# Performance work log

Measured on AMD Instinct MI355X. Metric: run time of the kernel, lower is better.

The kernel has to match this reference:

```python
import jax, jax.numpy as jnp
import numpy as np

DIM = 1024
HEADS = 16


def setup_inputs() -> dict:
    key = jax.random.key(0)
    ks = jax.random.split(key, 9)
    B, N, C = 2, 2048, DIM
    hd = C // HEADS
    s = 1.0 / np.sqrt(C)
    x = jax.random.normal(ks[0], (B, N, C), dtype=jnp.float32)
    wq = jax.random.normal(ks[1], (C, C), dtype=jnp.float32) * s
    wk = jax.random.normal(ks[2], (C, C), dtype=jnp.float32) * s
    wv = jax.random.normal(ks[3], (C, C), dtype=jnp.float32) * s
    wp = jax.random.normal(ks[4], (C, C), dtype=jnp.float32) * s
    bp = jnp.zeros((C,), dtype=jnp.float32)
    # rotary table: angles theta_j = 10000^{-2j/hd}, positions 0..N-1
    inv_freq = 1.0 / (10000.0 ** (jnp.arange(0, hd, 2, dtype=jnp.float32) / hd))
    ang = jnp.arange(N, dtype=jnp.float32)[:, None] * inv_freq[None, :]  # (N, hd//2)
    cos = jnp.cos(ang)
    sin = jnp.sin(ang)
    return {"x": x, "wq": wq, "wk": wk, "wv": wv, "wp": wp, "bp": bp,
            "cos": cos, "sin": sin, "num_heads": HEADS}


def _apply_rotary(t, cos, sin):
    # t: (B, N, H, D); cos/sin: (N, D//2) -> broadcast (1, N, 1, D//2)
    B, N, H, D = t.shape
    tr = t.reshape(B, N, H, D // 2, 2)
    t1, t2 = tr[..., 0], tr[..., 1]
    c = cos[None, :, None, :]
    s = sin[None, :, None, :]
    o1 = t1 * c - t2 * s
    o2 = t1 * s + t2 * c
    return jnp.stack([o1, o2], axis=-1).reshape(B, N, H, D)


def reference(x, wq, wk, wv, wp, bp, cos, sin, num_heads):
    B, N, C = x.shape
    H = num_heads
    D = C // H
    q = (x @ wq.T).reshape(B, N, H, D)
    k = (x @ wk.T).reshape(B, N, H, D)
    v = (x @ wv.T).reshape(B, N, H, D)
    q = _apply_rotary(q, cos, sin)
    k = _apply_rotary(k, cos, sin)
    scale = 1.0 / jnp.sqrt(jnp.asarray(D, dtype=x.dtype))
    # scores: (B, H, N, N)
    scores = jnp.einsum('bnhd,bmhd->bhnm', q, k) * scale
    attn = jax.nn.softmax(scores, axis=-1)
    out = jnp.einsum('bhnm,bmhd->bnhd', attn, v).reshape(B, N, C)
    return out @ wp.T + bp
```

## Files before the change

kernel.cpp:

```cpp
#include <hip/hip_runtime.h>
#include <hip/hip_bf16.h>
#include <stdint.h>

#define DEVI __device__ __forceinline__

using bf16 = __hip_bfloat16;
typedef __bf16 bf16x8 __attribute__((ext_vector_type(8)));
typedef __bf16 bf16x4 __attribute__((ext_vector_type(4)));
typedef float f32x4 __attribute__((ext_vector_type(4)));
typedef float f32x16 __attribute__((ext_vector_type(16)));
typedef int i32x2 __attribute__((ext_vector_type(2)));

static constexpr int Bb = 2, Nn = 2048, Cc = 1024, Hh = 16, Dd = 64;
static constexpr float CSC = 0.125f * 1.44269504088896340736f;

DEVI bf16 f2bf(float x) {
  __bf16 h = (__bf16)x;
  return *(bf16*)&h;
}
DEVI float fexp2(float x) { return __builtin_amdgcn_exp2f(x); }

DEVI bf16x8 cvt8(f32x4 a, f32x4 b) {
  bf16x8 r;
  r[0] = (__bf16)a[0]; r[1] = (__bf16)a[1]; r[2] = (__bf16)a[2]; r[3] = (__bf16)a[3];
  r[4] = (__bf16)b[0]; r[5] = (__bf16)b[1]; r[6] = (__bf16)b[2]; r[7] = (__bf16)b[3];
  return r;
}

DEVI uint32_t pk2(float a, float b) {
  __bf16 x = (__bf16)a, y = (__bf16)b;
  uint16_t ux = *(uint16_t*)&x, uy = *(uint16_t*)&y;
  return (uint32_t)ux | ((uint32_t)uy << 16);
}

DEVI bf16x8 mk8(uint32_t a, uint32_t b, uint32_t c, uint32_t d) {
  union { uint32_t u[4]; bf16x8 v; } x;
  x.u[0] = a; x.u[1] = b; x.u[2] = c; x.u[3] = d;
  return x.v;
}

DEVI void gld_lds16(const bf16* g, bf16* l) {
  __builtin_amdgcn_global_load_lds(
      (__attribute__((address_space(1))) void*)(g),
      (__attribute__((address_space(3))) void*)(l),
      16, 0, 0);
}

__global__ __launch_bounds__(256) void k_cvt(const float* __restrict__ x,
                                             const float* __restrict__ wq,
                                             const float* __restrict__ wk,
                                             const float* __restrict__ wv,
                                             const float* __restrict__ wp,
                                             bf16* xb, bf16* wqb, bf16* wkb,
                                             bf16* wvb, bf16* wpb) {
  int bid = blockIdx.x;
  const float* src; bf16* dst; size_t off;
  if (bid < 2048) {
    src = x; dst = xb; off = (size_t)bid * 2048;
  } else {
    int s = (bid - 2048) >> 9, r = (bid - 2048) & 511;
    off = (size_t)r * 2048;
    src = s == 0 ? wq : s == 1 ? wk : s == 2 ? wv : wp;
    dst = s == 0 ? wqb : s == 1 ? wkb : s == 2 ? wvb : wpb;
  }
  size_t i = off + (size_t)threadIdx.x * 8;
  f32x4 a = *(const f32x4*)(src + i);
  f32x4 b = *(const f32x4*)(src + i + 4);
  *(bf16x8*)(dst + i) = cvt8(a, b);
}

template <int MFC, class Epi>
DEVI void gemm_dbuf(const bf16* __restrict__ A, const bf16* __restrict__ Bw,
                    int K, int m0, int n0, bf16* lA, bf16* lB, Epi epi) {
  constexpr int BM = MFC * 32;
  constexpr int PA = BM / 64;
  constexpr int ASZ = BM * 32, BSZ = 128 * 32;
  const int t = threadIdx.x;
  const int lane = t & 63, wave = t >> 6, g = lane >> 4;
  const int wr = wave >> 1, wc = wave & 1;

  auto stage = [&](int k0, int buf) {
#pragma unroll
    for (int p = 0; p < PA; ++p) {
      int c = p * 256 + t;
      gld_lds16(A + (size_t)(m0 + (c >> 2)) * K + k0 + (c & 3) * 8,
                lA + buf * ASZ + (size_t)(p * 256 + wave * 64) * 8);
    }
#pragma unroll
    for (int p = 0; p < 2; ++p) {
      int c = p * 256 + t;
      gld_lds16(Bw + (size_t)(n0 + (c >> 2)) * K + k0 + (c & 3) * 8,
                lB + buf * BSZ + (size_t)(p * 256 + wave * 64) * 8);
    }
  };

  f32x4 acc[MFC][4] = {};
  stage(0, 0);
  __syncthreads();

  const int NS = K / 32;
  for (int s = 0; s < NS; ++s) {
    const int cur = s & 1;
    if (s + 1 < NS) stage((s + 1) * 32, cur ^ 1);

    bf16x8 aF[MFC];
#pragma unroll
    for (int mf = 0; mf < MFC; ++mf)
      aF[mf] = *(const bf16x8*)(lA + cur * ASZ +
                                (wr * (BM / 2) + mf * 16 + (lane & 15)) * 32 + g * 8);
#pragma unroll
    for (int nf = 0; nf < 4; ++nf) {
      bf16x8 bF = *(const bf16x8*)(lB + cur * BSZ +
                                   (wc * 64 + nf * 16 + (lane & 15)) * 32 + g * 8);
#pragma unroll
      for (int mf = 0; mf < MFC; ++mf)
        acc[mf][nf] = __builtin_amdgcn_mfma_f32_16x16x32_bf16(aF[mf], bF, acc[mf][nf], 0, 0, 0);
    }
    __syncthreads();
  }

#pragma unroll
  for (int mf = 0; mf < MFC; ++mf)
#pragma unroll
    for (int nf = 0; nf < 4; ++nf)
#pragma unroll
      for (int r = 0; r < 4; ++r) {
        int gm = m0 + wr * (BM / 2) + mf * 16 + g * 4 + r;
        int gn = n0 + wc * 64 + nf * 16 + (lane & 15);
        epi(gm, gn, acc[mf][nf][r]);
      }
}

struct EpiRope {
  bf16* dst; const float* cosw; const float* sinw; float scale;
  DEVI void operator()(int gm, int gn, float v) const {
    int b = gm >> 11, n = gm & 2047;
    int h = gn >> 6, d = gn & 63;
    int i = d >> 1;
    float c = cosw[n * 32 + i], s = sinw[n * 32 + i];
    float p = __shfl_xor(v, 1);
    float o = (d & 1) ? (p * s + v * c) : (v * c - p * s);
    dst[((size_t)(b * Hh + h) * Nn + n) * 64 + d] = f2bf(o * scale);
  }
};

struct EpiVt {
  bf16* dst;
  DEVI void operator()(int gm, int gn, float v) const {
    int h = gm >> 6, d = gm & 63;
    int b = gn >> 11, n = gn & 2047;
    dst[((size_t)(b * Hh + h) * 64 + d) * Nn + n] = f2bf(v);
  }
};

struct EpiProj {
  float* dst; const float* bias;
  DEVI void operator()(int gm, int gn, float v) const {
    dst[(size_t)gm * Cc + gn] = v + bias[gn];
  }
};

__global__ __launch_bounds__(256) void k_qkv(const bf16* __restrict__ xb,
                                             const bf16* __restrict__ wqb,
                                             const bf16* __restrict__ wkb,
                                             const bf16* __restrict__ wvb,
                                             bf16* q_ws, bf16* k_ws, bf16* vt_ws,
                                             const float* __restrict__ cw,
                                             const float* __restrict__ sw) {
  __shared__ __align__(16) bf16 lA[2 * 128 * 32];
  __shared__ __align__(16) bf16 lB[2 * 128 * 32];
  int bid = blockIdx.x;
  if (bid < 512) {
    int sub = bid & 255;
    int m0 = (sub >> 3) * 128, n0 = (sub & 7) * 128;
    bool isq = bid < 256;
    gemm_dbuf<4>(xb, isq ? wqb : wkb, Cc, m0, n0, lA, lB,
                 EpiRope{isq ? q_ws : k_ws, cw, sw, isq ? CSC : 1.0f});
  } else {
    int sub = bid - 512;
    int m0 = (sub & 7) * 128, n0 = (sub >> 3) * 128;
    gemm_dbuf<4>(wvb, xb, Cc, m0, n0, lA, lB, EpiVt{vt_ws});
  }
}

__global__ __launch_bounds__(256) void k_proj(const bf16* __restrict__ A,
                                              const bf16* __restrict__ W,
                                              float* dst, const float* __restrict__ bias) {
  __shared__ __align__(16) bf16 lA[2 * 64 * 32];
  __shared__ __align__(16) bf16 lB[2 * 128 * 32];
  gemm_dbuf<2>(A, W, Cc, blockIdx.x * 64, blockIdx.y * 128, lA, lB,
               EpiProj{dst, bias});
}

__global__ __launch_bounds__(256) void k_flash(const bf16* __restrict__ q_ws,
                                               const bf16* __restrict__ k_ws,
                                               const bf16* __restrict__ vt_ws,
                                               bf16* __restrict__ attn_o) {
  __shared__ __align__(16) bf16 lK[2][64 * 64];
  __shared__ __align__(16) bf16 lV[2][64 * 64];

  const int t = threadIdx.x, lane = t & 63, wave = t >> 6;
  const int l31 = lane & 31, hi = lane >> 5;
  const int bh = blockIdx.y;
  const int q0w = blockIdx.x * 128 + wave * 32;
  const bf16* qg = q_ws + (size_t)bh * Nn * 64;
  const bf16* kg = k_ws + (size_t)bh * Nn * 64;
  const bf16* vg = vt_ws + (size_t)bh * 64 * Nn;

  bf16x8 qF[4];
#pragma unroll
  for (int kd = 0; kd < 4; ++kd)
    qF[kd] = *(const bf16x8*)(qg + (size_t)(q0w + l31) * 64 + kd * 16 + hi * 8);

  f32x16 accO[2] = {};
  float LsL = 0.f;

  auto stage_tile = [&](int kt, int buf) {
#pragma unroll
    for (int p = 0; p < 2; ++p) {
      int c = p * 256 + t;
      int row = c >> 3, cis = (c & 7) ^ (row & 7);
      gld_lds16(kg + (size_t)(kt * 64 + row) * 64 + cis * 8,
                lK[buf] + (size_t)(p * 256 + wave * 64) * 8);
      gld_lds16(vg + (size_t)row * Nn + kt * 64 + cis * 8,
                lV[buf] + (size_t)(p * 256 + wave * 64) * 8);
    }
  };

  stage_tile(0, 0);
  __syncthreads();

  constexpr int NT = Nn / 64;
  for (int kt = 0; kt < NT; ++kt) {
    const int cur = kt & 1;
    if (kt + 1 < NT) stage_tile(kt + 1, cur ^ 1);

#pragma unroll
    for (int kb = 0; kb < 2; ++kb) {
      f32x16 accT = {};
      __builtin_amdgcn_s_setprio(1);
#pragma unroll
      for (int kd = 0; kd < 4; ++kd) {
        int row = kb * 32 + l31;
        bf16x8 kF = *(const bf16x8*)(lK[cur] +
            ((row * 64 + kd * 16 + hi * 8) ^ ((row & 7) << 3)));
        accT = __builtin_amdgcn_mfma_f32_32x32x16_bf16(kF, qF[kd], accT, 0, 0, 0);
      }
      __builtin_amdgcn_s_setprio(0);

      float p[16];
#pragma unroll
      for (int r = 0; r < 16; ++r) { p[r] = fexp2(accT[r]); LsL += p[r]; }

      uint32_t c01 = pk2(p[0], p[1]),  c23 = pk2(p[2], p[3]);
      uint32_t c89 = pk2(p[4], p[5]),  cab = pk2(p[6], p[7]);
      uint32_t d01 = pk2(p[8], p[9]),  d23 = pk2(p[10], p[11]);
      uint32_t d89 = pk2(p[12], p[13]), dab = pk2(p[14], p[15]);
      i32x2 s0a = __builtin_amdgcn_permlane32_swap((int)c01, (int)c89, false, false);
      i32x2 s0b = __builtin_amdgcn_permlane32_swap((int)c23, (int)cab, false, false);
      i32x2 s1a = __builtin_amdgcn_permlane32_swap((int)d01, (int)d89, false, false);
      i32x2 s1b = __builtin_amdgcn_permlane32_swap((int)d23, (int)dab, false, false);
      bf16x8 paF[2] = { mk8(s0a[0], s0b[0], s0a[1], s0b[1]),
                        mk8(s1a[0], s1b[0], s1a[1], s1b[1]) };

      __builtin_amdgcn_s_setprio(1);
#pragma unroll
      for (int d0 = 0; d0 < 2; ++d0) {
#pragma unroll
        for (int s = 0; s < 2; ++s) {
          int vrow = d0 * 32 + l31;
          bf16x8 vF = *(const bf16x8*)(lV[cur] +
              ((vrow * 64 + kb * 32 + s * 16 + hi * 8) ^ ((vrow & 7) << 3)));
          accO[d0] = __builtin_amdgcn_mfma_f32_32x32x16_bf16(paF[s], vF, accO[d0], 0, 0, 0);
        }
      }
      __builtin_amdgcn_s_setprio(0);
    }

    __syncthreads();
  }

  float L = LsL + __shfl_xor(LsL, 32);

  const int b = bh >> 4, h = bh & 15;
#pragma unroll
  for (int r = 0; r < 16; ++r) {
    int ql = (r & 3) + 8 * (r >> 2) + 4 * hi;
    float inv = 1.0f / __shfl(L, ql);
    int qrow = q0w + ql;
#pragma unroll
    for (int d0 = 0; d0 < 2; ++d0) {
      int d = d0 * 32 + l31;
      attn_o[((size_t)(b * Nn + qrow)) * Cc + h * 64 + d] = f2bf(accO[d0][r] * inv);
    }
  }
}

extern "C" void kernel_launch(void* const* d_in, const int* in_sizes, int n_in,
                              void* d_out, int out_size, void* d_ws, size_t ws_size,
                              hipStream_t stream) {
  (void)in_sizes; (void)n_in; (void)out_size; (void)ws_size;
  const float* x  = (const float*)d_in[0];
  const float* wq = (const float*)d_in[1];
  const float* wk = (const float*)d_in[2];
  const float* wv = (const float*)d_in[3];
  const float* wp = (const float*)d_in[4];
  const float* bp = (const float*)d_in[5];
  const float* cw = (const float*)d_in[6];
  const float* sw = (const float*)d_in[7];
  float* out = (float*)d_out;

  const size_t M1 = 1u << 20;
  bf16* x_bf  = (bf16*)d_ws;
  bf16* wq_bf = x_bf + 4 * M1;
  bf16* wk_bf = wq_bf + M1;
  bf16* wv_bf = wk_bf + M1;
  bf16* wp_bf = wv_bf + M1;
  bf16* q_ws  = wp_bf + M1;
  bf16* k_ws  = q_ws + 4 * M1;
  bf16* vt_ws = k_ws + 4 * M1;
  bf16* ao_ws = x_bf;

  k_cvt  <<<dim3(4096),    dim3(256), 0, stream>>>(x, wq, wk, wv, wp,
                                                   x_bf, wq_bf, wk_bf, wv_bf, wp_bf);
  k_qkv  <<<dim3(768),     dim3(256), 0, stream>>>(x_bf, wq_bf, wk_bf, wv_bf,
                                                   q_ws, k_ws, vt_ws, cw, sw);
  k_flash<<<dim3(16, 32),  dim3(256), 0, stream>>>(q_ws, k_ws, vt_ws, ao_ws);
  k_proj <<<dim3(64, 8),   dim3(256), 0, stream>>>(ao_ws, wp_bf, out, bp);
}
```

Baseline: 132.6 us.

## Reshape flash attention tiles and switch GEMMs to single-buffered LDS

The flash kernel now runs 128-thread blocks in which each wave handles 64 query rows as two 32-row sub-blocks, so each K/V fragment read from LDS feeds twice as many MFMAs. Blocks are remapped onto a 1D grid with a head-grouping swizzle. The row-sum accumulators are split four ways to shorten dependency chains. The GEMM helper drops double buffering in favour of one buffer with two barriers per k-step, and the QKV block indices are remapped, presumably for L2 locality. Halving the staging buffers cuts LDS use and may raise occupancy, but it loses the overlap of global loads with MFMA work.

```diff
diff --git a/kernel.cpp b/kernel.cpp
--- a/kernel.cpp
+++ b/kernel.cpp
@@ -6,7 +6,6 @@
 
 using bf16 = __hip_bfloat16;
 typedef __bf16 bf16x8 __attribute__((ext_vector_type(8)));
-typedef __bf16 bf16x4 __attribute__((ext_vector_type(4)));
 typedef float f32x4 __attribute__((ext_vector_type(4)));
 typedef float f32x16 __attribute__((ext_vector_type(16)));
 typedef int i32x2 __attribute__((ext_vector_type(2)));
@@ -14,10 +13,7 @@
 static constexpr int Bb = 2, Nn = 2048, Cc = 1024, Hh = 16, Dd = 64;
 static constexpr float CSC = 0.125f * 1.44269504088896340736f;
 
-DEVI bf16 f2bf(float x) {
-  __bf16 h = (__bf16)x;
-  return *(bf16*)&h;
-}
+DEVI bf16 f2bf(float x) { __bf16 h = (__bf16)x; return *(bf16*)&h; }
 DEVI float fexp2(float x) { return __builtin_amdgcn_exp2f(x); }
 
 DEVI bf16x8 cvt8(f32x4 a, f32x4 b) {
@@ -70,53 +66,45 @@
 }
 
 template <int MFC, class Epi>
-DEVI void gemm_dbuf(const bf16* __restrict__ A, const bf16* __restrict__ Bw,
-                    int K, int m0, int n0, bf16* lA, bf16* lB, Epi epi) {
+DEVI void gemm_lds_body(const bf16* __restrict__ A, const bf16* __restrict__ Bw,
+                        int K, int m0, int n0, bf16* lA, bf16* lB, Epi epi) {
   constexpr int BM = MFC * 32;
   constexpr int PA = BM / 64;
-  constexpr int ASZ = BM * 32, BSZ = 128 * 32;
   const int t = threadIdx.x;
-  const int lane = t & 63, wave = t >> 6, g = lane >> 4;
+  const int lane = t & 63, wave = t >> 6;
   const int wr = wave >> 1, wc = wave & 1;
 
-  auto stage = [&](int k0, int buf) {
+  f32x4 acc[MFC][4] = {};
+
+  for (int k0 = 0; k0 < K; k0 += 32) {
+    __syncthreads();
 #pragma unroll
     for (int p = 0; p < PA; ++p) {
       int c = p * 256 + t;
-      gld_lds16(A + (size_t)(m0 + (c >> 2)) * K + k0 + (c & 3) * 8,
-                lA + buf * ASZ + (size_t)(p * 256 + wave * 64) * 8);
+      int row = c >> 2, col = (c & 3) * 8;
+      gld_lds16(A + (size_t)(m0 + row) * K + k0 + col,
+                lA + (size_t)(p * 256 + wave * 64) * 8);
     }
 #pragma unroll
     for (int p = 0; p < 2; ++p) {
       int c = p * 256 + t;
-      gld_lds16(Bw + (size_t)(n0 + (c >> 2)) * K + k0 + (c & 3) * 8,
-                lB + buf * BSZ + (size_t)(p * 256 + wave * 64) * 8);
-    }
-  };
-
-  f32x4 acc[MFC][4] = {};
-  stage(0, 0);
-  __syncthreads();
-
-  const int NS = K / 32;
-  for (int s = 0; s < NS; ++s) {
-    const int cur = s & 1;
-    if (s + 1 < NS) stage((s + 1) * 32, cur ^ 1);
+      int row = c >> 2, col = (c & 3) * 8;
+      gld_lds16(Bw + (size_t)(n0 + row) * K + k0 + col,
+                lB + (size_t)(p * 256 + wave * 64) * 8);
+    }
+    __syncthreads();
 
     bf16x8 aF[MFC];
 #pragma unroll
     for (int mf = 0; mf < MFC; ++mf)
-      aF[mf] = *(const bf16x8*)(lA + cur * ASZ +
-                                (wr * (BM / 2) + mf * 16 + (lane & 15)) * 32 + g * 8);
+      aF[mf] = *(const bf16x8*)(lA + (wr * (BM / 2) + mf * 16 + (lane & 15)) * 32 + (lane >> 4) * 8);
 #pragma unroll
     for (int nf = 0; nf < 4; ++nf) {
-      bf16x8 bF = *(const bf16x8*)(lB + cur * BSZ +
-                                   (wc * 64 + nf * 16 + (lane & 15)) * 32 + g * 8);
+      bf16x8 bF = *(const bf16x8*)(lB + (wc * 64 + nf * 16 + (lane & 15)) * 32 + (lane >> 4) * 8);
 #pragma unroll
       for (int mf = 0; mf < MFC; ++mf)
         acc[mf][nf] = __builtin_amdgcn_mfma_f32_16x16x32_bf16(aF[mf], bF, acc[mf][nf], 0, 0, 0);
     }
-    __syncthreads();
   }
 
 #pragma unroll
@@ -125,7 +113,7 @@
     for (int nf = 0; nf < 4; ++nf)
 #pragma unroll
       for (int r = 0; r < 4; ++r) {
-        int gm = m0 + wr * (BM / 2) + mf * 16 + g * 4 + r;
+        int gm = m0 + wr * (BM / 2) + mf * 16 + (lane >> 4) * 4 + r;
         int gn = n0 + wc * 64 + nf * 16 + (lane & 15);
         epi(gm, gn, acc[mf][nf][r]);
       }
@@ -167,32 +155,36 @@
                                              bf16* q_ws, bf16* k_ws, bf16* vt_ws,
                                              const float* __restrict__ cw,
                                              const float* __restrict__ sw) {
-  __shared__ __align__(16) bf16 lA[2 * 128 * 32];
-  __shared__ __align__(16) bf16 lB[2 * 128 * 32];
+  __shared__ __align__(16) bf16 smem[256 * 32];
+  bf16* lA = smem;
+  bf16* lB = smem + 128 * 32;
   int bid = blockIdx.x;
   if (bid < 512) {
     int sub = bid & 255;
-    int m0 = (sub >> 3) * 128, n0 = (sub & 7) * 128;
+    int c = sub & 7, rest = sub >> 3;
+    int m0 = (c + 8 * (rest & 3)) * 128;
+    int n0 = (rest >> 2) * 128;
     bool isq = bid < 256;
-    gemm_dbuf<4>(xb, isq ? wqb : wkb, Cc, m0, n0, lA, lB,
-                 EpiRope{isq ? q_ws : k_ws, cw, sw, isq ? CSC : 1.0f});
+    gemm_lds_body<4>(xb, isq ? wqb : wkb, Cc, m0, n0, lA, lB,
+                     EpiRope{isq ? q_ws : k_ws, cw, sw, isq ? CSC : 1.0f});
   } else {
     int sub = bid - 512;
-    int m0 = (sub & 7) * 128, n0 = (sub >> 3) * 128;
-    gemm_dbuf<4>(wvb, xb, Cc, m0, n0, lA, lB, EpiVt{vt_ws});
+    int c = sub & 7, rest = sub >> 3;
+    int n0 = (c + 8 * (rest & 3)) * 128;
+    int m0 = (rest >> 2) * 128;
+    gemm_lds_body<4>(wvb, xb, Cc, m0, n0, lA, lB, EpiVt{vt_ws});
   }
 }
 
 __global__ __launch_bounds__(256) void k_proj(const bf16* __restrict__ A,
                                               const bf16* __restrict__ W,
                                               float* dst, const float* __restrict__ bias) {
-  __shared__ __align__(16) bf16 lA[2 * 64 * 32];
-  __shared__ __align__(16) bf16 lB[2 * 128 * 32];
-  gemm_dbuf<2>(A, W, Cc, blockIdx.x * 64, blockIdx.y * 128, lA, lB,
-               EpiProj{dst, bias});
-}
-
-__global__ __launch_bounds__(256) void k_flash(const bf16* __restrict__ q_ws,
+  __shared__ __align__(16) bf16 smem[192 * 32];
+  gemm_lds_body<2>(A, W, Cc, blockIdx.x * 64, blockIdx.y * 128,
+                   smem, smem + 64 * 32, EpiProj{dst, bias});
+}
+
+__global__ __launch_bounds__(128) void k_flash(const bf16* __restrict__ q_ws,
                                                const bf16* __restrict__ k_ws,
                                                const bf16* __restrict__ vt_ws,
                                                bf16* __restrict__ attn_o) {
@@ -201,29 +193,33 @@
 
   const int t = threadIdx.x, lane = t & 63, wave = t >> 6;
   const int l31 = lane & 31, hi = lane >> 5;
-  const int bh = blockIdx.y;
-  const int q0w = blockIdx.x * 128 + wave * 32;
+  const int bid = blockIdx.x;
+  const int slot = bid >> 3;
+  const int bh = (bid & 7) * 4 + (slot >> 4);
+  const int q0w = (slot & 15) * 128 + wave * 64;
   const bf16* qg = q_ws + (size_t)bh * Nn * 64;
   const bf16* kg = k_ws + (size_t)bh * Nn * 64;
   const bf16* vg = vt_ws + (size_t)bh * 64 * Nn;
 
-  bf16x8 qF[4];
-#pragma unroll
-  for (int kd = 0; kd < 4; ++kd)
-    qF[kd] = *(const bf16x8*)(qg + (size_t)(q0w + l31) * 64 + kd * 16 + hi * 8);
-
-  f32x16 accO[2] = {};
-  float LsL = 0.f;
+  bf16x8 qF[2][4];
+#pragma unroll
+  for (int qb = 0; qb < 2; ++qb)
+#pragma unroll
+    for (int kd = 0; kd < 4; ++kd)
+      qF[qb][kd] = *(const bf16x8*)(qg + (size_t)(q0w + qb * 32 + l31) * 64 + kd * 16 + hi * 8);
+
+  f32x16 accO[2][2] = {};
+  float Ls4[2][4] = {};
 
   auto stage_tile = [&](int kt, int buf) {
 #pragma unroll
-    for (int p = 0; p < 2; ++p) {
-      int c = p * 256 + t;
+    for (int p = 0; p < 4; ++p) {
+      int c = p * 128 + t;
       int row = c >> 3, cis = (c & 7) ^ (row & 7);
       gld_lds16(kg + (size_t)(kt * 64 + row) * 64 + cis * 8,
-                lK[buf] + (size_t)(p * 256 + wave * 64) * 8);
+                lK[buf] + (size_t)(p * 128 + wave * 64) * 8);
       gld_lds16(vg + (size_t)row * Nn + kt * 64 + cis * 8,
-                lV[buf] + (size_t)(p * 256 + wave * 64) * 8);
+                lV[buf] + (size_t)(p * 128 + wave * 64) * 8);
     }
   };
 
@@ -237,61 +233,76 @@
 
 #pragma unroll
     for (int kb = 0; kb < 2; ++kb) {
-      f32x16 accT = {};
-      __builtin_amdgcn_s_setprio(1);
+      bf16x8 kF[4];
 #pragma unroll
       for (int kd = 0; kd < 4; ++kd) {
         int row = kb * 32 + l31;
-        bf16x8 kF = *(const bf16x8*)(lK[cur] +
+        kF[kd] = *(const bf16x8*)(lK[cur] +
             ((row * 64 + kd * 16 + hi * 8) ^ ((row & 7) << 3)));
-        accT = __builtin_amdgcn_mfma_f32_32x32x16_bf16(kF, qF[kd], accT, 0, 0, 0);
       }
-      __builtin_amdgcn_s_setprio(0);
-
-      float p[16];
-#pragma unroll
-      for (int r = 0; r < 16; ++r) { p[r] = fexp2(accT[r]); LsL += p[r]; }
-
-      uint32_t c01 = pk2(p[0], p[1]),  c23 = pk2(p[2], p[3]);
-      uint32_t c89 = pk2(p[4], p[5]),  cab = pk2(p[6], p[7]);
-      uint32_t d01 = pk2(p[8], p[9]),  d23 = pk2(p[10], p[11]);
-      uint32_t d89 = pk2(p[12], p[13]), dab = pk2(p[14], p[15]);
-      i32x2 s0a = __builtin_amdgcn_permlane32_swap((int)c01, (int)c89, false, false);
-      i32x2 s0b = __builtin_amdgcn_permlane32_swap((int)c23, (int)cab, false, false);
-      i32x2 s1a = __builtin_amdgcn_permlane32_swap((int)d01, (int)d89, false, false);
-      i32x2 s1b = __builtin_amdgcn_permlane32_swap((int)d23, (int)dab, false, false);
-      bf16x8 paF[2] = { mk8(s0a[0], s0b[0], s0a[1], s0b[1]),
-                        mk8(s1a[0], s1b[0], s1a[1], s1b[1]) };
-
-      __builtin_amdgcn_s_setprio(1);
-#pragma unroll
-      for (int d0 = 0; d0 < 2; ++d0) {
+      bf16x8 vF[2][2];
+#pragma unroll
+      for (int d0 = 0; d0 < 2; ++d0)
 #pragma unroll
         for (int s = 0; s < 2; ++s) {
           int vrow = d0 * 32 + l31;
-          bf16x8 vF = *(const bf16x8*)(lV[cur] +
+          vF[d0][s] = *(const bf16x8*)(lV[cur] +
               ((vrow * 64 + kb * 32 + s * 16 + hi * 8) ^ ((vrow & 7) << 3)));
-          accO[d0] = __builtin_amdgcn_mfma_f32_32x32x16_bf16(paF[s], vF, accO[d0], 0, 0, 0);
         }
+
+#pragma unroll
+      for (int qb = 0; qb < 2; ++qb) {
+        f32x16 accT = {};
+        __builtin_amdgcn_s_setprio(1);
+#pragma unroll
+        for (int kd = 0; kd < 4; ++kd)
+          accT = __builtin_amdgcn_mfma_f32_32x32x16_bf16(kF[kd], qF[qb][kd], accT, 0, 0, 0);
+        __builtin_amdgcn_s_setprio(0);
+
+        float p[16];
+#pragma unroll
+        for (int r = 0; r < 16; ++r) { p[r] = fexp2(accT[r]); Ls4[qb][r & 3] += p[r]; }
+
+        uint32_t c01 = pk2(p[0], p[1]),  c23 = pk2(p[2], p[3]);
+        uint32_t c89 = pk2(p[4], p[5]),  cab = pk2(p[6], p[7]);
+        uint32_t d01 = pk2(p[8], p[9]),  d23 = pk2(p[10], p[11]);
+        uint32_t d89 = pk2(p[12], p[13]), dab = pk2(p[14], p[15]);
+        i32x2 s0a = __builtin_amdgcn_permlane32_swap((int)c01, (int)c89, false, false);
+        i32x2 s0b = __builtin_amdgcn_permlane32_swap((int)c23, (int)cab, false, false);
+        i32x2 s1a = __builtin_amdgcn_permlane32_swap((int)d01, (int)d89, false, false);
+        i32x2 s1b = __builtin_amdgcn_permlane32_swap((int)d23, (int)dab, false, false);
+        bf16x8 paF[2] = { mk8(s0a[0], s0b[0], s0a[1], s0b[1]),
+                          mk8(s1a[0], s1b[0], s1a[1], s1b[1]) };
+
+        __builtin_amdgcn_s_setprio(1);
+#pragma unroll
+        for (int d0 = 0; d0 < 2; ++d0)
+#pragma unroll
+          for (int s = 0; s < 2; ++s)
+            accO[qb][d0] = __builtin_amdgcn_mfma_f32_32x32x16_bf16(paF[s], vF[d0][s], accO[qb][d0], 0, 0, 0);
+        __builtin_amdgcn_s_setprio(0);
       }
-      __builtin_amdgcn_s_setprio(0);
     }
 
     __syncthreads();
   }
 
-  float L = LsL + __shfl_xor(LsL, 32);
-
   const int b = bh >> 4, h = bh & 15;
 #pragma unroll
-  for (int r = 0; r < 16; ++r) {
-    int ql = (r & 3) + 8 * (r >> 2) + 4 * hi;
-    float inv = 1.0f / __shfl(L, ql);
-    int qrow = q0w + ql;
-#pragma unroll
-    for (int d0 = 0; d0 < 2; ++d0) {
-      int d = d0 * 32 + l31;
-      attn_o[((size_t)(b * Nn + qrow)) * Cc + h * 64 + d] = f2bf(accO[d0][r] * inv);
+  for (int qb = 0; qb < 2; ++qb) {
+    float L = (Ls4[qb][0] + Ls4[qb][1]) + (Ls4[qb][2] + Ls4[qb][3]);
+    L += __shfl_xor(L, 32);
+
+#pragma unroll
+    for (int r = 0; r < 16; ++r) {
+      int ql = (r & 3) + 8 * (r >> 2) + 4 * hi;
+      float inv = 1.0f / __shfl(L, ql);
+      int qrow = q0w + qb * 32 + ql;
+#pragma unroll
+      for (int d0 = 0; d0 < 2; ++d0) {
+        int d = d0 * 32 + l31;
+        attn_o[((size_t)(b * Nn + qrow)) * Cc + h * 64 + d] = f2bf(accO[qb][d0][r] * inv);
+      }
     }
   }
 }
@@ -325,6 +336,6 @@
                                                    x_bf, wq_bf, wk_bf, wv_bf, wp_bf);
   k_qkv  <<<dim3(768),     dim3(256), 0, stream>>>(x_bf, wq_bf, wk_bf, wv_bf,
                                                    q_ws, k_ws, vt_ws, cw, sw);
-  k_flash<<<dim3(16, 32),  dim3(256), 0, stream>>>(q_ws, k_ws, vt_ws, ao_ws);
+  k_flash<<<dim3(512),     dim3(128), 0, stream>>>(q_ws, k_ws, vt_ws, ao_ws);
   k_proj <<<dim3(64, 8),   dim3(256), 0, stream>>>(ao_ws, wp_bf, out, bp);
 }
```

Result: slower. 163.1 us (+23.0%).
